# Performance work log

Hardware: AMD Instinct MI355X
Metric: run time of the kernel (lower is better)

## Reference

```python
import jax, jax.numpy as jnp
import numpy as np

# Hardware-emulation constants (from init_kwargs, NeuroSim-style QLinear)
WL_IN = 8        # input activation bit width (bit-serial)
WL_W = 8         # weight bit width
CELL_BIT = 2     # bits per memory cell -> 4 weight slices
SUB = 128        # crossbar sub-array size (rows summed in analog)
ADC_BITS = 5     # ADC precision per partial sum
ONOFF = 10.0     # cell on/off conductance ratio
VARI = 0.05      # multiplicative device variation sigma


def _adc_quant(x, bits, axes):
    # LinearQuantizeOut: uniform quantization between tensor min/max
    mn = jnp.min(x, axis=axes, keepdims=True)
    mx = jnp.max(x, axis=axes, keepdims=True)
    step = (mx - mn) * (2.0 ** (-bits))
    step = jnp.where(step <= 0, 1.0, step)
    idx = jnp.clip(jnp.floor((x - mn) / step), 0.0, 2.0 ** bits - 1.0)
    return idx * step + mn


def _qlinear_hw(x, w, noise):
    """Analog PIM crossbar emulation of y = x @ w.T with bit-serial inputs,
    bit-sliced cells, on/off-ratio offset + dummy column, device variation,
    per-subarray ADC quantization."""
    B, N = x.shape
    F = w.shape[0]
    I, W, K = WL_IN, WL_W, WL_W // CELL_BIT
    cr = 2.0 ** CELL_BIT
    lower, upper = 1.0 / ONOFF, 1.0
    S = (N + SUB - 1) // SUB
    Np = S * SUB
    # quantize input to I bits in [0,1]; weight to W-bit integer in [0, 2^W-1]
    xq = jnp.round(jnp.clip(x, 0.0, 1.0) * (2.0 ** I - 1.0))            # [B, N]
    Xi = jnp.clip(jnp.round((w + 1.0) * 0.5 * (2.0 ** W - 1.0)), 0.0, 2.0 ** W - 1.0)  # [F, N]
    xq = jnp.pad(xq, ((0, 0), (0, Np - N)))
    Xi = jnp.pad(Xi, ((0, 0), (0, Np - N)))
    zpow = 2.0 ** jnp.arange(I, dtype=x.dtype)
    kpow = cr ** jnp.arange(K, dtype=x.dtype)
    bits = jnp.mod(jnp.floor(xq[..., None] / zpow), 2.0)                # [B, Np, I]
    slc = jnp.mod(jnp.floor(Xi[..., None] / kpow), cr)                  # [F, Np, K]
    g = slc * (upper - lower) + (cr - 1.0) * lower                      # cell conductances
    g = g * (1.0 + VARI * noise)                                        # device variation
    bits = bits.reshape(B, S, SUB, I)
    g = g.reshape(F, S, SUB, K)
    # analog partial sums per (input bit i, subarray s, weight slice k)
    P = jnp.einsum('bsai,fsak->iskbf', bits, g)                         # [I,S,K,B,F]
    # dummy column (all cells at lowest conductance), identical across F
    D = jnp.transpose(bits.sum(axis=2), (2, 1, 0)) * ((cr - 1.0) * lower)  # [I,S,B]
    Pq = _adc_quant(P, ADC_BITS, axes=(3, 4))
    Dq = _adc_quant(D, ADC_BITS, axes=(2,))
    scal = (2.0 ** jnp.arange(I, dtype=x.dtype))[:, None] * (cr ** jnp.arange(K, dtype=x.dtype))[None, :]
    acc = jnp.einsum('iskbf,ik->bf', Pq - Dq[:, :, None, :, None], scal) / (upper - lower)
    # undo integer mappings: w = 2*Xi/(2^W-1) - 1, x = xq/(2^I-1)
    out = 2.0 * acc / ((2.0 ** I - 1.0) * (2.0 ** W - 1.0)) \
          - xq.sum(axis=1, keepdims=True) / (2.0 ** I - 1.0)
    return out


def _qlinear(x, w, noise):
    # straight-through quantized weight (WAGE-style STE) + hardware forward
    Xi = jnp.clip(jnp.round((w + 1.0) * 0.5 * (2.0 ** WL_W - 1.0)), 0.0, 2.0 ** WL_W - 1.0)
    wq = 2.0 * Xi / (2.0 ** WL_W - 1.0) - 1.0
    wq_ste = w + jax.lax.stop_gradient(wq - w)
    out_ideal = x @ wq_ste.T
    out_hw = _qlinear_hw(x, w, noise)
    return out_ideal + jax.lax.stop_gradient(out_hw - out_ideal)


def setup_inputs() -> dict:
    key = jax.random.key(0)
    k1, k2, k3, k4, k5 = jax.random.split(key, 5)
    x = jax.random.uniform(k1, (1024, 784), dtype=jnp.float32)
    w1 = jax.random.normal(k2, (512, 784), dtype=jnp.float32) * 0.05
    w3 = jax.random.normal(k3, (10, 512), dtype=jnp.float32) * 0.08
    noise1 = jax.random.normal(k4, (512, 896, 4), dtype=jnp.float32)  # 784 padded to 7*128
    noise3 = jax.random.normal(k5, (10, 512, 4), dtype=jnp.float32)   # 512 = 4*128 exact
    return {"x": x, "w1": w1, "w3": w3, "noise1": noise1, "noise3": noise3}


def reference(x, w1, w3, noise1, noise3):
    h = jnp.tanh(_qlinear(x, w1, noise1))   # QLinear(784,512) + Tanh
    return _qlinear(h, w3, noise3)          # QLinear(512,10)
```

## Files before the change

kernel.cpp:

```cpp
#include <hip/hip_runtime.h>

#define FLTMAX 3.402823466e+38f


__global__ void init_kernel(float* __restrict__ acc1, unsigned* __restrict__ stats1)
{
    int gid = blockIdx.x * 256 + threadIdx.x;
    if (gid < 1024 * 512) acc1[gid] = 0.f;
    if (gid < 224) { stats1[gid * 2] = 0x7F7FFFFFu; stats1[gid * 2 + 1] = 0u; }
}

__global__ void prep1_kernel(const float* __restrict__ x, float* __restrict__ xq1,
                             float* __restrict__ sx1)
{
    __shared__ float red[128];
    int b = blockIdx.x;
    float psum = 0.f;
    for (int n = threadIdx.x; n < 896; n += 128) {
        float v = 0.f;
        if (n < 784) {
            float xv = x[b * 784 + n];
            xv = fminf(fmaxf(xv, 0.f), 1.f);
            v = rintf(__fmul_rn(xv, 255.f));
        }
        xq1[b * 896 + n] = v;
        psum += v;
    }
    red[threadIdx.x] = psum;
    __syncthreads();
    for (int w = 64; w >= 1; w >>= 1) {
        if (threadIdx.x < w) red[threadIdx.x] += red[threadIdx.x + w];
        __syncthreads();
    }
    if (threadIdx.x == 0) sx1[b] = red[0];
}

__global__ void prepg1t_kernel(const float* __restrict__ w1, const float* __restrict__ noise1,
                               float* __restrict__ g1t)
{
    __shared__ float t[4][32][33];
    const int n0 = blockIdx.x * 32, f0 = blockIdx.y * 32;
    const int tid = threadIdx.x;
    {
        int n = tid & 31, fi = tid >> 5;
#pragma unroll
        for (int p = 0; p < 4; ++p) {
            int f = p * 8 + fi;
            int gn = n0 + n, gf = f0 + f;
            float gv[4] = {0.f, 0.f, 0.f, 0.f};
            if (gn < 784) {
                float w = w1[gf * 784 + gn];
                float Xi = fminf(fmaxf(rintf(__fmul_rn(__fmul_rn(__fadd_rn(w, 1.f), 0.5f), 255.f)),
                                       0.f), 255.f);
                int xi = (int)Xi;
                float4 nz = *(const float4*)&noise1[(gf * 896 + gn) * 4];
                float nzv[4] = {nz.x, nz.y, nz.z, nz.w};
#pragma unroll
                for (int k = 0; k < 4; ++k) {
                    int slc = (xi >> (2 * k)) & 3;
                    float base = __fadd_rn(__fmul_rn((float)slc, 0.9f), 0.3f);
                    float nf = __fadd_rn(1.f, __fmul_rn(0.05f, nzv[k]));
                    gv[k] = __fmul_rn(base, nf);
                }
            }
#pragma unroll
            for (int k = 0; k < 4; ++k) t[k][n][f] = gv[k];
        }
    }
    __syncthreads();
    {
        int f = tid & 31, nn = tid >> 5;
#pragma unroll
        for (int p = 0; p < 4; ++p) {
            int n = p * 8 + nn;
#pragma unroll
            for (int k = 0; k < 4; ++k)
                g1t[(n0 + n) * 2048 + k * 512 + f0 + f] = t[k][n][f];
        }
    }
}

__global__ void transpose_kernel(const float* __restrict__ in, float* __restrict__ out,
                                 int R, int C)
{
    __shared__ float tile[32][33];
    int c0 = blockIdx.x * 32, r0 = blockIdx.y * 32;
    int tx = threadIdx.x & 31, ty4 = (threadIdx.x >> 5) * 4;
#pragma unroll
    for (int u = 0; u < 4; ++u)
        tile[ty4 + u][tx] = in[(r0 + ty4 + u) * C + c0 + tx];
    __syncthreads();
#pragma unroll
    for (int u = 0; u < 4; ++u)
        out[(c0 + ty4 + u) * R + r0 + tx] = tile[tx][ty4 + u];
}

__global__ void prepg2_kernel(const float* __restrict__ w3, const float* __restrict__ noise3,
                              float* __restrict__ g2t)
{
    int gid = blockIdx.x * 256 + threadIdx.x;
    if (gid >= 10 * 512) return;
    int f = gid / 512, n = gid % 512;
    float w = w3[f * 512 + n];
    float Xi = fminf(fmaxf(rintf(__fmul_rn(__fmul_rn(__fadd_rn(w, 1.f), 0.5f), 255.f)),
                           0.f), 255.f);
    int xi = (int)Xi;
#pragma unroll
    for (int k = 0; k < 4; ++k) {
        int slc = (xi >> (2 * k)) & 3;
        float base = __fadd_rn(__fmul_rn((float)slc, 0.9f), 0.3f);
        float nf = __fadd_rn(1.f, __fmul_rn(0.05f, noise3[(f * 512 + n) * 4 + k]));
        g2t[n * 40 + k * 10 + f] = __fmul_rn(base, nf);
    }
}

__global__ void dq_kernel(const float* __restrict__ xq, float* __restrict__ Dq,
                          int S, int rowstride)
{
    __shared__ float red[512];
    const int i = blockIdx.x / S, s = blockIdx.x % S;
    const int tid = threadIdx.x;
    float D[4];
    float mn = FLTMAX, mx = -FLTMAX;
#pragma unroll
    for (int u = 0; u < 4; ++u) {
        int b = tid + u * 256;
        const float4* row = (const float4*)&xq[b * rowstride + s * 128];
        int c = 0;
#pragma unroll 8
        for (int q = 0; q < 32; ++q) {
            float4 v = row[q];
            c += (((int)v.x >> i) & 1) + (((int)v.y >> i) & 1) +
                 (((int)v.z >> i) & 1) + (((int)v.w >> i) & 1);
        }
        D[u] = __fmul_rn((float)c, 0.3f);
        mn = fminf(mn, D[u]);
        mx = fmaxf(mx, D[u]);
    }
    red[tid] = mn; red[256 + tid] = mx;
    __syncthreads();
    for (int w = 128; w >= 1; w >>= 1) {
        if (tid < w) {
            red[tid] = fminf(red[tid], red[tid + w]);
            red[256 + tid] = fmaxf(red[256 + tid], red[256 + tid + w]);
        }
        __syncthreads();
    }
    mn = red[0]; mx = red[256];
    float step = __fmul_rn(__fsub_rn(mx, mn), 0.03125f);
    if (step <= 0.f) step = 1.f;
#pragma unroll
    for (int u = 0; u < 4; ++u) {
        int b = tid + u * 256;
        float idx = fminf(fmaxf(floorf(__fdiv_rn(__fsub_rn(D[u], mn), step)), 0.f), 31.f);
        Dq[(i * S + s) * 1024 + b] = __fadd_rn(__fmul_rn(idx, step), mn);
    }
}

__global__ void dterm_kernel(const float* __restrict__ Dq, float* __restrict__ dterm, int S)
{
    int b = blockIdx.x * 256 + threadIdx.x;
    if (b >= 1024) return;
    float sum = 0.f;
    for (int i = 0; i < 8; ++i) {
        float sc = (float)(85 << i);
        for (int s = 0; s < S; ++s) sum = fmaf(Dq[(i * S + s) * 1024 + b], sc, sum);
    }
    dterm[b] = sum;
}

#define BK 32
__global__ __launch_bounds__(256, 2) void mm1_kernel(
    const float* __restrict__ xqT, const float* __restrict__ g1t,
    float* __restrict__ P, unsigned* __restrict__ stats, int s, int i0)
{
    __shared__ __align__(16) float As[BK][256];
    __shared__ __align__(16) float Bs[BK][128];
    __shared__ float red[512];
    const int tid = threadIdx.x;
    const int row0 = blockIdx.x * 256;
    const int i = i0 + (row0 >> 10);
    const int b0 = row0 & 1023;
    const int colBase = blockIdx.y * 128;
    const int nbase = s * 128;
    const int tx = tid & 15, ty = tid >> 4;

    const int aA = tid >> 6;
    const int eA = (tid & 63) << 2;
    const int aB = tid >> 5;
    const int eB = (tid & 31) << 2;

    float4 pA[8], pB[4];
#pragma unroll
    for (int u = 0; u < 8; ++u)
        pA[u] = *(const float4*)&xqT[(nbase + u * 4 + aA) * 1024 + b0 + eA];
#pragma unroll
    for (int u = 0; u < 4; ++u)
        pB[u] = *(const float4*)&g1t[(nbase + u * 8 + aB) * 2048 + colBase + eB];

    float acc[16][8] = {};

    for (int ac = 0; ac < 4; ++ac) {
        __syncthreads();
#pragma unroll
        for (int u = 0; u < 8; ++u) {
            float4 av = pA[u];
            float4 ab;
            ab.x = (float)((((int)av.x) >> i) & 1);
            ab.y = (float)((((int)av.y) >> i) & 1);
            ab.z = (float)((((int)av.z) >> i) & 1);
            ab.w = (float)((((int)av.w) >> i) & 1);
            *(float4*)&As[u * 4 + aA][eA] = ab;
        }
#pragma unroll
        for (int u = 0; u < 4; ++u)
            *(float4*)&Bs[u * 8 + aB][eB] = pB[u];
        __syncthreads();

        if (ac < 3) {
            const int n0 = nbase + (ac + 1) * BK;
#pragma unroll
            for (int u = 0; u < 8; ++u)
                pA[u] = *(const float4*)&xqT[(n0 + u * 4 + aA) * 1024 + b0 + eA];
#pragma unroll
            for (int u = 0; u < 4; ++u)
                pB[u] = *(const float4*)&g1t[(n0 + u * 8 + aB) * 2048 + colBase + eB];
        }

#pragma unroll 2
        for (int a = 0; a < BK; ++a) {
            float ar[16], br[8];
            *(float4*)&ar[0]  = *(const float4*)&As[a][(ty << 2)];
            *(float4*)&ar[4]  = *(const float4*)&As[a][64 + (ty << 2)];
            *(float4*)&ar[8]  = *(const float4*)&As[a][128 + (ty << 2)];
            *(float4*)&ar[12] = *(const float4*)&As[a][192 + (ty << 2)];
            *(float4*)&br[0]  = *(const float4*)&Bs[a][(tx << 2)];
            *(float4*)&br[4]  = *(const float4*)&Bs[a][64 + (tx << 2)];
#pragma unroll
            for (int u = 0; u < 16; ++u)
#pragma unroll
                for (int v = 0; v < 8; ++v)
                    acc[u][v] = fmaf(ar[u], br[v], acc[u][v]);
        }
    }

#pragma unroll
    for (int q = 0; q < 4; ++q)
#pragma unroll
        for (int u = 0; u < 4; ++u) {
            int row = row0 + q * 64 + (ty << 2) + u;
#pragma unroll
            for (int vh = 0; vh < 2; ++vh) {
                float4 v = make_float4(acc[q * 4 + u][vh * 4 + 0], acc[q * 4 + u][vh * 4 + 1],
                                       acc[q * 4 + u][vh * 4 + 2], acc[q * 4 + u][vh * 4 + 3]);
                *(float4*)&P[(size_t)row * 2048 + colBase + vh * 64 + (tx << 2)] = v;
            }
        }

    float mn = acc[0][0], mx = acc[0][0];
#pragma unroll
    for (int u = 0; u < 16; ++u)
#pragma unroll
        for (int v = 0; v < 8; ++v) { mn = fminf(mn, acc[u][v]); mx = fmaxf(mx, acc[u][v]); }
    red[tid] = mn; red[256 + tid] = mx;
    __syncthreads();
    for (int w = 128; w >= 1; w >>= 1) {
        if (tid < w) {
            red[tid] = fminf(red[tid], red[tid + w]);
            red[256 + tid] = fmaxf(red[256 + tid], red[256 + tid + w]);
        }
        __syncthreads();
    }
    if (tid == 0) {
        int k = colBase >> 9;
        int slot = ((s * 8 + i) * 4 + k) * 2;
        atomicMin(&stats[slot], __float_as_uint(red[0]));
        atomicMax(&stats[slot + 1], __float_as_uint(red[256]));
    }
}

__global__ void quant1_kernel(const float* __restrict__ P, const unsigned* __restrict__ stats,
                              float* __restrict__ acc1, int s, int i0, int ni)
{
    int gid = blockIdx.x * 256 + threadIdx.x;
    int b = gid >> 7, f4 = gid & 127;
    float4 sum = make_float4(0.f, 0.f, 0.f, 0.f);
    for (int il = 0; il < ni; ++il) {
        int i = i0 + il;
#pragma unroll
        for (int k = 0; k < 4; ++k) {
            int slot = ((s * 8 + i) * 4 + k) * 2;
            float mn = __uint_as_float(stats[slot]);
            float mx = __uint_as_float(stats[slot + 1]);
            float step = __fmul_rn(__fsub_rn(mx, mn), 0.03125f);
            if (step <= 0.f) step = 1.f;
            float4 val = *(const float4*)&P[(size_t)(il * 1024 + b) * 2048 + (k << 9) + (f4 << 2)];
            float sc = (float)(1 << (i + 2 * k));
            float ix, pq;
            ix = fminf(fmaxf(floorf(__fdiv_rn(__fsub_rn(val.x, mn), step)), 0.f), 31.f);
            pq = __fadd_rn(__fmul_rn(ix, step), mn); sum.x = fmaf(pq, sc, sum.x);
            ix = fminf(fmaxf(floorf(__fdiv_rn(__fsub_rn(val.y, mn), step)), 0.f), 31.f);
            pq = __fadd_rn(__fmul_rn(ix, step), mn); sum.y = fmaf(pq, sc, sum.y);
            ix = fminf(fmaxf(floorf(__fdiv_rn(__fsub_rn(val.z, mn), step)), 0.f), 31.f);
            pq = __fadd_rn(__fmul_rn(ix, step), mn); sum.z = fmaf(pq, sc, sum.z);
            ix = fminf(fmaxf(floorf(__fdiv_rn(__fsub_rn(val.w, mn), step)), 0.f), 31.f);
            pq = __fadd_rn(__fmul_rn(ix, step), mn); sum.w = fmaf(pq, sc, sum.w);
        }
    }
    float4* ap = (float4*)&acc1[(b << 9) + (f4 << 2)];
    float4 a = *ap;
    a.x += sum.x; a.y += sum.y; a.z += sum.z; a.w += sum.w;
    *ap = a;
}

__global__ void finish1_kernel(const float* __restrict__ acc1, const float* __restrict__ dterm1,
                               const float* __restrict__ sx1, float* __restrict__ xq2)
{
    int gid = blockIdx.x * 256 + threadIdx.x;
    int b = gid >> 9;
    float total = __fsub_rn(acc1[gid], dterm1[b]);
    float acc = __fdiv_rn(total, 0.9f);
    float o = __fsub_rn(__fdiv_rn(__fmul_rn(2.f, acc), 65025.f), __fdiv_rn(sx1[b], 255.f));
    float h = tanhf(o);
    h = fminf(fmaxf(h, 0.f), 1.f);
    xq2[gid] = rintf(__fmul_rn(h, 255.f));
}

__global__ void sx2_kernel(const float* __restrict__ xq2, float* __restrict__ sx2)
{
    __shared__ float red[128];
    int b = blockIdx.x;
    float psum = 0.f;
    for (int n = threadIdx.x; n < 512; n += 128) psum += xq2[b * 512 + n];
    red[threadIdx.x] = psum;
    __syncthreads();
    for (int w = 64; w >= 1; w >>= 1) {
        if (threadIdx.x < w) red[threadIdx.x] += red[threadIdx.x + w];
        __syncthreads();
    }
    if (threadIdx.x == 0) sx2[b] = red[0];
}

__global__ void mm2_kernel(const float* __restrict__ xq2, const float* __restrict__ g2t,
                           float* __restrict__ P2)
{
    int gid = blockIdx.x * 256 + threadIdx.x;
    if (gid >= 40960) return;
    int f = gid % 10;
    int b = (gid / 10) & 1023;
    int s = gid / 10240;
    float acc[8][4] = {};
    for (int a = 0; a < 128; ++a) {
        int n = s * 128 + a;
        int xi = (int)xq2[b * 512 + n];
        float g0 = g2t[n * 40 + f];
        float gA = g2t[n * 40 + 10 + f];
        float gB = g2t[n * 40 + 20 + f];
        float gC = g2t[n * 40 + 30 + f];
#pragma unroll
        for (int i = 0; i < 8; ++i) {
            float bi = (float)((xi >> i) & 1);
            acc[i][0] = fmaf(bi, g0, acc[i][0]);
            acc[i][1] = fmaf(bi, gA, acc[i][1]);
            acc[i][2] = fmaf(bi, gB, acc[i][2]);
            acc[i][3] = fmaf(bi, gC, acc[i][3]);
        }
    }
#pragma unroll
    for (int i = 0; i < 8; ++i)
#pragma unroll
        for (int k = 0; k < 4; ++k)
            P2[(size_t)((s * 8 + i) * 4 + k) * 10240 + b * 10 + f] = acc[i][k];
}

__global__ void stat2_kernel(const float* __restrict__ P2, float2* __restrict__ stats2)
{
    __shared__ float red[512];
    int p = blockIdx.x;
    int tid = threadIdx.x;
    float mn = FLTMAX, mx = -FLTMAX;
    for (int t = tid; t < 10240; t += 256) {
        float v = P2[(size_t)p * 10240 + t];
        mn = fminf(mn, v); mx = fmaxf(mx, v);
    }
    red[tid] = mn; red[256 + tid] = mx;
    __syncthreads();
    for (int w = 128; w >= 1; w >>= 1) {
        if (tid < w) {
            red[tid] = fminf(red[tid], red[tid + w]);
            red[256 + tid] = fmaxf(red[256 + tid], red[256 + tid + w]);
        }
        __syncthreads();
    }
    if (tid == 0) {
        float step = __fmul_rn(__fsub_rn(red[256], red[0]), 0.03125f);
        if (step <= 0.f) step = 1.f;
        stats2[p] = make_float2(red[0], step);
    }
}

__global__ void out2_kernel(const float* __restrict__ P2, const float2* __restrict__ stats2,
                            const float* __restrict__ dterm2, const float* __restrict__ sx2,
                            float* __restrict__ out)
{
    int gid = blockIdx.x * 256 + threadIdx.x;
    if (gid >= 10240) return;
    int b = gid / 10;
    float sum = 0.f;
    for (int s = 0; s < 4; ++s)
        for (int i = 0; i < 8; ++i)
#pragma unroll
            for (int k = 0; k < 4; ++k) {
                int p = (s * 8 + i) * 4 + k;
                float2 st = stats2[p];
                float val = P2[(size_t)p * 10240 + gid];
                float idx = fminf(fmaxf(floorf(__fdiv_rn(__fsub_rn(val, st.x), st.y)), 0.f), 31.f);
                float pq = __fadd_rn(__fmul_rn(idx, st.y), st.x);
                sum = fmaf(pq, (float)(1 << (i + 2 * k)), sum);
            }
    float total = __fsub_rn(sum, dterm2[b]);
    float acc = __fdiv_rn(total, 0.9f);
    out[gid] = __fsub_rn(__fdiv_rn(__fmul_rn(2.f, acc), 65025.f), __fdiv_rn(sx2[b], 255.f));
}

extern "C" void kernel_launch(void* const* d_in, const int* in_sizes, int n_in,
                              void* d_out, int out_size, void* d_ws, size_t ws_size,
                              hipStream_t stream)
{
    const float* x      = (const float*)d_in[0];
    const float* w1     = (const float*)d_in[1];
    const float* w3     = (const float*)d_in[2];
    const float* noise1 = (const float*)d_in[3];
    const float* noise3 = (const float*)d_in[4];
    float* out = (float*)d_out;
    float* ws  = (float*)d_ws;

    float*    xq1    = ws + 0;
    float*    g1t    = ws + 917504;
    float*    acc1   = ws + 2752512;
    float*    xq2    = ws + 3276800;
    float*    P2     = ws + 3801088;
    float*    g2t    = ws + 5111808;
    float*    Dq1    = ws + 5132288;
    float*    Dq2    = ws + 5189632;
    float*    sx1    = ws + 5222400;
    float*    sx2    = ws + 5223424;
    float*    dterm1 = ws + 5224448;
    float*    dterm2 = ws + 5225472;
    float2*   stats2 = (float2*)(ws + 5226496);
    unsigned* stats1 = (unsigned*)(ws + 5226752);
    float*    xqT    = ws + 5227264;
    float*    Ps     = ws + 6144768;

    const size_t fixedf = 6144768;
    int ni = 8;
    while (ni > 1 && (fixedf + (size_t)ni * 2097152) * sizeof(float) > ws_size) ni >>= 1;

    init_kernel<<<2048, 256, 0, stream>>>(acc1, stats1);
    prep1_kernel<<<1024, 128, 0, stream>>>(x, xq1, sx1);
    prepg1t_kernel<<<dim3(28, 16), 256, 0, stream>>>(w1, noise1, g1t);
    transpose_kernel<<<dim3(28, 32), 256, 0, stream>>>(xq1, xqT, 1024, 896);
    dq_kernel<<<56, 256, 0, stream>>>(xq1, Dq1, 7, 896);
    dterm_kernel<<<4, 256, 0, stream>>>(Dq1, dterm1, 7);

    for (int s = 0; s < 7; ++s)
        for (int i0 = 0; i0 < 8; i0 += ni) {
            mm1_kernel<<<dim3(4 * ni, 16), 256, 0, stream>>>(xqT, g1t, Ps, stats1, s, i0);
            quant1_kernel<<<512, 256, 0, stream>>>(Ps, stats1, acc1, s, i0, ni);
        }

    finish1_kernel<<<2048, 256, 0, stream>>>(acc1, dterm1, sx1, xq2);
    sx2_kernel<<<1024, 128, 0, stream>>>(xq2, sx2);
    prepg2_kernel<<<20, 256, 0, stream>>>(w3, noise3, g2t);
    dq_kernel<<<32, 256, 0, stream>>>(xq2, Dq2, 4, 512);
    dterm_kernel<<<4, 256, 0, stream>>>(Dq2, dterm2, 4);
    mm2_kernel<<<160, 256, 0, stream>>>(xq2, g2t, P2);
    stat2_kernel<<<128, 256, 0, stream>>>(P2, stats2);
    out2_kernel<<<40, 256, 0, stream>>>(P2, stats2, dterm2, sx2, out);
}
```

Baseline: 704.0 us.

## Bit-pack input bit-planes and drop float transpose in layer-1 crossbar matmul

Replaces the float transposed input with a precomputed bit-packed layout: each 32-element chunk of each row is stored as one 32-bit word per input bit. mm1 then loads one word per row per K-chunk and extracts bits in registers, instead of staging a 256x32 float A tile in shared memory. The row tile drops from 256 to 128, so the grid doubles, and launch bounds rise to 4 blocks per SM. Shared-memory and global A traffic fall sharply, at the cost of extra shift/convert ALU work per FMA and less register reuse of each B fragment.

```diff
diff --git a/kernel.cpp b/kernel.cpp
--- a/kernel.cpp
+++ b/kernel.cpp
@@ -33,6 +33,23 @@
         __syncthreads();
     }
     if (threadIdx.x == 0) sx1[b] = red[0];
+}
+
+__global__ void bitpack_kernel(const float* __restrict__ xq1, unsigned* __restrict__ xqb)
+{
+    int gid = blockIdx.x * 256 + threadIdx.x;
+    if (gid >= 1024 * 28) return;
+    int b = gid / 28, w = gid % 28;
+    unsigned words[8] = {0, 0, 0, 0, 0, 0, 0, 0};
+    const float* src = &xq1[b * 896 + w * 32];
+#pragma unroll 8
+    for (int n = 0; n < 32; ++n) {
+        int v = (int)src[n];
+#pragma unroll
+        for (int i = 0; i < 8; ++i) words[i] |= ((unsigned)((v >> i) & 1)) << n;
+    }
+#pragma unroll
+    for (int i = 0; i < 8; ++i) xqb[(i * 1024 + b) * 28 + w] = words[i];
 }
 
 __global__ void prepg1t_kernel(const float* __restrict__ w1, const float* __restrict__ noise1,
@@ -80,21 +97,6 @@
     }
 }
 
-__global__ void transpose_kernel(const float* __restrict__ in, float* __restrict__ out,
-                                 int R, int C)
-{
-    __shared__ float tile[32][33];
-    int c0 = blockIdx.x * 32, r0 = blockIdx.y * 32;
-    int tx = threadIdx.x & 31, ty4 = (threadIdx.x >> 5) * 4;
-#pragma unroll
-    for (int u = 0; u < 4; ++u)
-        tile[ty4 + u][tx] = in[(r0 + ty4 + u) * C + c0 + tx];
-    __syncthreads();
-#pragma unroll
-    for (int u = 0; u < 4; ++u)
-        out[(c0 + ty4 + u) * R + r0 + tx] = tile[tx][ty4 + u];
-}
-
 __global__ void prepg2_kernel(const float* __restrict__ w3, const float* __restrict__ noise3,
                               float* __restrict__ g2t)
 {
@@ -170,96 +172,86 @@
 }
 
 #define BK 32
-__global__ __launch_bounds__(256, 2) void mm1_kernel(
-    const float* __restrict__ xqT, const float* __restrict__ g1t,
+__global__ __launch_bounds__(256, 4) void mm1_kernel(
+    const unsigned* __restrict__ xqb, const float* __restrict__ g1t,
     float* __restrict__ P, unsigned* __restrict__ stats, int s, int i0)
 {
-    __shared__ __align__(16) float As[BK][256];
-    __shared__ __align__(16) float Bs[BK][128];
+    __shared__ __align__(16) float Bs[BK][132];
+    __shared__ unsigned Abits[128];
     __shared__ float red[512];
     const int tid = threadIdx.x;
-    const int row0 = blockIdx.x * 256;
-    const int i = i0 + (row0 >> 10);
-    const int b0 = row0 & 1023;
+    const int il = blockIdx.x >> 3;
+    const int i = i0 + il;
+    const int b0 = (blockIdx.x & 7) * 128;
     const int colBase = blockIdx.y * 128;
-    const int nbase = s * 128;
     const int tx = tid & 15, ty = tid >> 4;
 
-    const int aA = tid >> 6;
-    const int eA = (tid & 63) << 2;
     const int aB = tid >> 5;
     const int eB = (tid & 31) << 2;
 
-    float4 pA[8], pB[4];
-#pragma unroll
-    for (int u = 0; u < 8; ++u)
-        pA[u] = *(const float4*)&xqT[(nbase + u * 4 + aA) * 1024 + b0 + eA];
+    float4 pB[4];
+    unsigned pAw = 0;
 #pragma unroll
     for (int u = 0; u < 4; ++u)
-        pB[u] = *(const float4*)&g1t[(nbase + u * 8 + aB) * 2048 + colBase + eB];
-
-    float acc[16][8] = {};
+        pB[u] = *(const float4*)&g1t[(s * 128 + u * 8 + aB) * 2048 + colBase + eB];
+    if (tid < 128) pAw = xqb[(i * 1024 + b0 + tid) * 28 + s * 4];
+
+    float acc[8][8] = {};
 
     for (int ac = 0; ac < 4; ++ac) {
         __syncthreads();
-#pragma unroll
-        for (int u = 0; u < 8; ++u) {
-            float4 av = pA[u];
-            float4 ab;
-            ab.x = (float)((((int)av.x) >> i) & 1);
-            ab.y = (float)((((int)av.y) >> i) & 1);
-            ab.z = (float)((((int)av.z) >> i) & 1);
-            ab.w = (float)((((int)av.w) >> i) & 1);
-            *(float4*)&As[u * 4 + aA][eA] = ab;
-        }
 #pragma unroll
         for (int u = 0; u < 4; ++u)
             *(float4*)&Bs[u * 8 + aB][eB] = pB[u];
+        if (tid < 128) Abits[tid] = pAw;
         __syncthreads();
 
         if (ac < 3) {
-            const int n0 = nbase + (ac + 1) * BK;
-#pragma unroll
-            for (int u = 0; u < 8; ++u)
-                pA[u] = *(const float4*)&xqT[(n0 + u * 4 + aA) * 1024 + b0 + eA];
+            const int n0 = s * 128 + (ac + 1) * BK;
 #pragma unroll
             for (int u = 0; u < 4; ++u)
                 pB[u] = *(const float4*)&g1t[(n0 + u * 8 + aB) * 2048 + colBase + eB];
-        }
-
-#pragma unroll 2
+            if (tid < 128) pAw = xqb[(i * 1024 + b0 + tid) * 28 + s * 4 + ac + 1];
+        }
+
+        unsigned wrd[8];
+#pragma unroll
+        for (int u = 0; u < 4; ++u) {
+            wrd[u]     = Abits[(ty << 2) + u];
+            wrd[4 + u] = Abits[64 + (ty << 2) + u];
+        }
+
+#pragma unroll 4
         for (int a = 0; a < BK; ++a) {
-            float ar[16], br[8];
-            *(float4*)&ar[0]  = *(const float4*)&As[a][(ty << 2)];
-            *(float4*)&ar[4]  = *(const float4*)&As[a][64 + (ty << 2)];
-            *(float4*)&ar[8]  = *(const float4*)&As[a][128 + (ty << 2)];
-            *(float4*)&ar[12] = *(const float4*)&As[a][192 + (ty << 2)];
-            *(float4*)&br[0]  = *(const float4*)&Bs[a][(tx << 2)];
-            *(float4*)&br[4]  = *(const float4*)&Bs[a][64 + (tx << 2)];
-#pragma unroll
-            for (int u = 0; u < 16; ++u)
+            float br[8];
+            *(float4*)&br[0] = *(const float4*)&Bs[a][(tx << 2)];
+            *(float4*)&br[4] = *(const float4*)&Bs[a][64 + (tx << 2)];
+#pragma unroll
+            for (int u = 0; u < 8; ++u) {
+                float ab = (float)((wrd[u] >> a) & 1u);
 #pragma unroll
                 for (int v = 0; v < 8; ++v)
-                    acc[u][v] = fmaf(ar[u], br[v], acc[u][v]);
-        }
-    }
-
-#pragma unroll
-    for (int q = 0; q < 4; ++q)
+                    acc[u][v] = fmaf(ab, br[v], acc[u][v]);
+            }
+        }
+    }
+
+#pragma unroll
+    for (int uh = 0; uh < 2; ++uh)
 #pragma unroll
         for (int u = 0; u < 4; ++u) {
-            int row = row0 + q * 64 + (ty << 2) + u;
+            int row = il * 1024 + b0 + uh * 64 + (ty << 2) + u;
 #pragma unroll
             for (int vh = 0; vh < 2; ++vh) {
-                float4 v = make_float4(acc[q * 4 + u][vh * 4 + 0], acc[q * 4 + u][vh * 4 + 1],
-                                       acc[q * 4 + u][vh * 4 + 2], acc[q * 4 + u][vh * 4 + 3]);
+                float4 v = make_float4(acc[uh * 4 + u][vh * 4 + 0], acc[uh * 4 + u][vh * 4 + 1],
+                                       acc[uh * 4 + u][vh * 4 + 2], acc[uh * 4 + u][vh * 4 + 3]);
                 *(float4*)&P[(size_t)row * 2048 + colBase + vh * 64 + (tx << 2)] = v;
             }
         }
 
     float mn = acc[0][0], mx = acc[0][0];
 #pragma unroll
-    for (int u = 0; u < 16; ++u)
+    for (int u = 0; u < 8; ++u)
 #pragma unroll
         for (int v = 0; v < 8; ++v) { mn = fminf(mn, acc[u][v]); mx = fmaxf(mx, acc[u][v]); }
     red[tid] = mn; red[256 + tid] = mx;
@@ -449,23 +441,23 @@
     float*    dterm2 = ws + 5225472;
     float2*   stats2 = (float2*)(ws + 5226496);
     unsigned* stats1 = (unsigned*)(ws + 5226752);
-    float*    xqT    = ws + 5227264;
-    float*    Ps     = ws + 6144768;
-
-    const size_t fixedf = 6144768;
+    unsigned* xqb    = (unsigned*)(ws + 5227264);
+    float*    Ps     = ws + 5456640;
+
+    const size_t fixedf = 5456640;
     int ni = 8;
     while (ni > 1 && (fixedf + (size_t)ni * 2097152) * sizeof(float) > ws_size) ni >>= 1;
 
     init_kernel<<<2048, 256, 0, stream>>>(acc1, stats1);
     prep1_kernel<<<1024, 128, 0, stream>>>(x, xq1, sx1);
     prepg1t_kernel<<<dim3(28, 16), 256, 0, stream>>>(w1, noise1, g1t);
-    transpose_kernel<<<dim3(28, 32), 256, 0, stream>>>(xq1, xqT, 1024, 896);
+    bitpack_kernel<<<112, 256, 0, stream>>>(xq1, xqb);
     dq_kernel<<<56, 256, 0, stream>>>(xq1, Dq1, 7, 896);
     dterm_kernel<<<4, 256, 0, stream>>>(Dq1, dterm1, 7);
 
     for (int s = 0; s < 7; ++s)
         for (int i0 = 0; i0 < 8; i0 += ni) {
-            mm1_kernel<<<dim3(4 * ni, 16), 256, 0, stream>>>(xqT, g1t, Ps, stats1, s, i0);
+            mm1_kernel<<<dim3(8 * ni, 16), 256, 0, stream>>>(xqb, g1t, Ps, stats1, s, i0);
             quant1_kernel<<<512, 256, 0, stream>>>(Ps, stats1, acc1, s, i0, ni);
         }
 
```

Result: slower. 757.8 us (+7.7%).
